# Kernel optimization log

Hardware: AMD Instinct MI355X
Metric: run time of the kernel (lower is better)

The kernel has to match this reference:

```python
import jax, jax.numpy as jnp
import numpy as np

B, N, D = 2, 2048, 1024
RANK, HEADS = 256, 16
HS = RANK // HEADS          # 16, low-rank head size for QK
DH = D // HEADS             # 64, value head size
SCALE = 1.0 / np.sqrt(HS)


def setup_inputs() -> dict:
    key = jax.random.key(0)
    k1, k2, k3 = jax.random.split(key, 3)
    x = jax.random.normal(k1, (B, N, D), dtype=jnp.float32)
    # causal additive mask, 0 on/below diag, -1e9 above
    mask = jnp.where(jnp.tril(jnp.ones((N, N), dtype=bool)), 0.0, -1e9).astype(jnp.float32)
    Wqk = jax.random.normal(k2, (2 * RANK, D), dtype=jnp.float32) * (1.0 / np.sqrt(D))
    Wv = jax.random.normal(k3, (D, D), dtype=jnp.float32) * (1.0 / np.sqrt(D))
    return {"x": x, "mask": mask, "Wqk": Wqk, "Wv": Wv}


def reference(x, mask, Wqk, Wv):
    b, n, d = x.shape
    qk = jnp.einsum('bnd,rd->bnr', x, Wqk)            # [b,n,2*rank]
    q, k = jnp.split(qk, 2, axis=-1)                  # [b,n,rank] each
    # L2 normalize over FULL rank dim (before head split), clamp norm >= 1e-6
    q = q / jnp.maximum(jnp.linalg.norm(q, axis=-1, keepdims=True), 1e-6)
    k = k / jnp.maximum(jnp.linalg.norm(k, axis=-1, keepdims=True), 1e-6)
    q = q.reshape(b, n, HEADS, HS).transpose(0, 2, 1, 3)   # [b,h,n,hs]
    k = k.reshape(b, n, HEADS, HS).transpose(0, 2, 1, 3)
    v = jnp.einsum('bnd,ed->bne', x, Wv).reshape(b, n, HEADS, DH).transpose(0, 2, 1, 3)  # [b,h,n,dh]
    att = jnp.einsum('bhqe,bhke->bhqk', q, k) * SCALE
    att = jnp.clip(att, -10000.0, 10000.0)
    att = att + mask[None, None, :, :]
    att = jax.nn.softmax(att, axis=-1)
    # NaN guard: zero NaNs then renormalize (no-op when no NaNs)
    att = jnp.where(jnp.isnan(att), 0.0, att)
    att = att / jnp.maximum(att.sum(axis=-1, keepdims=True), 1e-6)
    y = jnp.einsum('bhqk,bhkd->bhqd', att, v)              # [b,h,n,dh]
    return y.transpose(0, 2, 1, 3).reshape(b, n, d)
```

## Files before the change

### kernel.cpp

```cpp
#include <hip/hip_runtime.h>
#include <math.h>

#define BATCH 2
#define SEQ   2048
#define DIM   1024
#define RANK  256
#define HEADS 16
#define HS    16
#define DH    64
#define MROWS 4096

#define QSCALE 0.36067376f

typedef __attribute__((ext_vector_type(8)))  short    short8;
typedef __attribute__((ext_vector_type(4)))  float    f32x4;
typedef __attribute__((ext_vector_type(16))) float    f32x16;
typedef __attribute__((ext_vector_type(2)))  unsigned uint2v;

__device__ __forceinline__ unsigned short f2bf(float f) {
    union { float f; unsigned u; } v; v.f = f;
    return (unsigned short)((v.u + 0x7FFFu + ((v.u >> 16) & 1u)) >> 16);
}
__device__ __forceinline__ float bf2f(unsigned short h) {
    union { unsigned u; float f; } v; v.u = ((unsigned)h) << 16;
    return v.f;
}

#define XQ   1048576
#define WQKQ 131072
#define WVQ  262144
__global__ __launch_bounds__(256) void conv3(const float* __restrict__ x,
                                             const float* __restrict__ wqk,
                                             const float* __restrict__ wv,
                                             unsigned short* __restrict__ xb,
                                             unsigned short* __restrict__ wcat)
{
    const int i = blockIdx.x * 256 + threadIdx.x;
    const float* src; unsigned short* dst; int j;
    if (i < XQ)              { src = x;   dst = xb;   j = i; }
    else if (i < XQ + WQKQ)  { src = wqk; dst = wcat; j = i - XQ; }
    else                     { src = wv;  dst = wcat + (size_t)4 * WQKQ; j = i - XQ - WQKQ; }
    float4 v = ((const float4*)src)[j];
    ushort4 o; o.x = f2bf(v.x); o.y = f2bf(v.y); o.z = f2bf(v.z); o.w = f2bf(v.w);
    ((ushort4*)dst)[j] = o;
}

__global__ __launch_bounds__(256) void gemm_mfma(const unsigned short* __restrict__ A,
                                                 const unsigned short* __restrict__ W,
                                                 unsigned short* __restrict__ qkb,
                                                 unsigned short* __restrict__ vt)
{
    __shared__ __align__(16) unsigned short Alds[128 * 32];
    __shared__ __align__(16) unsigned short Blds[64 * 32];

    const int tid = threadIdx.x;
    const int w = tid >> 6, lane = tid & 63;
    const int lr = lane & 15, lg = lane >> 4;
    const int wm = w >> 1, wn = w & 1;
    const int bm = blockIdx.x * 128, bn = blockIdx.y * 64;

    const int srow = lane >> 2;
    const int sk   = (lane & 3) * 8;

    f32x4 acc[4][2] = {};

    for (int k0 = 0; k0 < 1024; k0 += 32) {
        __syncthreads();
        #pragma unroll
        for (int q = 0; q < 2; ++q) {
            const int r = (w * 2 + q) * 16 + srow;
            __builtin_amdgcn_global_load_lds(
                (const __attribute__((address_space(1))) unsigned int*)&A[(size_t)(bm + r) * 1024 + k0 + sk],
                (__attribute__((address_space(3))) unsigned int*)&Alds[(w * 2 + q) * 512],
                16, 0, 0);
        }
        __builtin_amdgcn_global_load_lds(
            (const __attribute__((address_space(1))) unsigned int*)&W[(size_t)(bn + w * 16 + srow) * 1024 + k0 + sk],
            (__attribute__((address_space(3))) unsigned int*)&Blds[w * 512],
            16, 0, 0);
        __syncthreads();

        short8 af[4], bfr[2];
        #pragma unroll
        for (int mi = 0; mi < 4; ++mi)
            af[mi] = *(const short8*)&Alds[(wm * 64 + mi * 16 + lr) * 32 + lg * 8];
        #pragma unroll
        for (int ni = 0; ni < 2; ++ni)
            bfr[ni] = *(const short8*)&Blds[(wn * 32 + ni * 16 + lr) * 32 + lg * 8];
        #pragma unroll
        for (int mi = 0; mi < 4; ++mi)
            #pragma unroll
            for (int ni = 0; ni < 2; ++ni)
                acc[mi][ni] = __builtin_amdgcn_mfma_f32_16x16x32_bf16(af[mi], bfr[ni], acc[mi][ni], 0, 0, 0);
    }

    if (bn < 512) {
        #pragma unroll
        for (int mi = 0; mi < 4; ++mi) {
            const int rbase = bm + wm * 64 + mi * 16 + lg * 4;
            #pragma unroll
            for (int ni = 0; ni < 2; ++ni) {
                const int col = bn + wn * 32 + ni * 16 + lr;
                #pragma unroll
                for (int r = 0; r < 4; ++r)
                    qkb[(size_t)(rbase + r) * 512 + col] = f2bf(acc[mi][ni][r]);
            }
        }
    } else {
        const int nb = bn - 512;
        #pragma unroll
        for (int mi = 0; mi < 4; ++mi) {
            const int m = bm + wm * 64 + mi * 16 + lg * 4;
            const int bb = m >> 11, ms = m & 2047;
            #pragma unroll
            for (int ni = 0; ni < 2; ++ni) {
                const int d = nb + wn * 32 + ni * 16 + lr;
                ushort4 pk;
                pk.x = f2bf(acc[mi][ni][0]); pk.y = f2bf(acc[mi][ni][1]);
                pk.z = f2bf(acc[mi][ni][2]); pk.w = f2bf(acc[mi][ni][3]);
                *(ushort4*)&vt[((size_t)bb * DIM + d) * SEQ + ms] = pk;
            }
        }
    }
}

__global__ __launch_bounds__(256) void l2norm_split(const unsigned short* __restrict__ qkb,
                                                    unsigned short* __restrict__ qn,
                                                    unsigned short* __restrict__ kn)
{
    const int row = blockIdx.x;
    const int t = threadIdx.x;
    const unsigned short* p = qkb + (size_t)row * 512;
    float q = bf2f(p[t]);
    float k = bf2f(p[t + 256]);
    float sq = q * q, sk = k * k;
    #pragma unroll
    for (int off = 32; off > 0; off >>= 1) {
        sq += __shfl_down(sq, off);
        sk += __shfl_down(sk, off);
    }
    __shared__ float sh[8];
    const int wid = t >> 6;
    if ((t & 63) == 0) { sh[wid * 2] = sq; sh[wid * 2 + 1] = sk; }
    __syncthreads();
    sq = sh[0] + sh[2] + sh[4] + sh[6];
    sk = sh[1] + sh[3] + sh[5] + sh[7];
    const float rq = QSCALE / fmaxf(sqrtf(sq), 1e-6f);
    const float rk = 1.0f   / fmaxf(sqrtf(sk), 1e-6f);
    qn[(size_t)row * 256 + t] = f2bf(q * rq);
    kn[(size_t)row * 256 + t] = f2bf(k * rk);
}


template<bool MASK>
__device__ __forceinline__ void tile32(const unsigned short* Vs, int keybase, int kh,
                                       int l31, int hi, int qg,
                                       const short8 ak0, const short8 ak1, const short8 bq,
                                       f32x16 o[2], float& lpart)
{
    const f32x16 z = {};
    const f32x16 s0 = __builtin_amdgcn_mfma_f32_32x32x16_bf16(ak0, bq, z, 0, 0, 0);
    const f32x16 s1 = __builtin_amdgcn_mfma_f32_32x32x16_bf16(ak1, bq, z, 0, 0, 0);

    float p0[16], p1[16];
    #pragma unroll
    for (int r = 0; r < 16; ++r) {
        float e0 = __builtin_exp2f(s0[r]);
        float e1 = __builtin_exp2f(s1[r]);
        if (MASK) {
            const int kl = keybase + (r & 3) + 8 * (r >> 2) + 4 * hi;
            e0 = (kl > qg) ? 0.0f : e0;
            e1 = (kl + 32 > qg) ? 0.0f : e1;
        }
        p0[r] = e0; p1[r] = e1;
        lpart += e0 + e1;
    }

    short8 pa[4];
    #pragma unroll
    for (int g = 0; g < 4; ++g) {
        const float* pc = (g < 2) ? p0 : p1;
        const int jj = 2 * (g & 1);
        unsigned a0, a1, b0, b1;
        asm("v_cvt_pk_bf16_f32 %0, %1, %2" : "=v"(a0) : "v"(pc[4*jj]),     "v"(pc[4*jj + 1]));
        asm("v_cvt_pk_bf16_f32 %0, %1, %2" : "=v"(b0) : "v"(pc[4*jj + 2]), "v"(pc[4*jj + 3]));
        asm("v_cvt_pk_bf16_f32 %0, %1, %2" : "=v"(a1) : "v"(pc[4*jj + 4]), "v"(pc[4*jj + 5]));
        asm("v_cvt_pk_bf16_f32 %0, %1, %2" : "=v"(b1) : "v"(pc[4*jj + 6]), "v"(pc[4*jj + 7]));
        const uint2v r0 = __builtin_amdgcn_permlane32_swap(a0, a1, false, false);
        const uint2v r1 = __builtin_amdgcn_permlane32_swap(b0, b1, false, false);
        union { short8 s; unsigned u[4]; } pu;
        pu.u[0] = r0[0]; pu.u[1] = r1[0]; pu.u[2] = r0[1]; pu.u[3] = r1[1];
        pa[g] = pu.s;
    }

    #pragma unroll
    for (int g = 0; g < 4; ++g)
        #pragma unroll
        for (int half = 0; half < 2; ++half) {
            const int row = half * 32 + l31;
            const short8 bv = *(const short8*)&Vs[row * 128 + ((64 * kh + 16 * g + 8 * hi) ^ (8 * (row & 7)))];
            o[half] = __builtin_amdgcn_mfma_f32_32x32x16_bf16(pa[g], bv, o[half], 0, 0, 0);
        }
}

__device__ __forceinline__ void seg_tile(const unsigned short* Vs, int kb, int kh,
                                         int l31, int hi, int qband, int qg, bool last,
                                         const short8 ak0, const short8 ak1, const short8 bq,
                                         f32x16 o[2], float& lpart)
{
    if (!last) {
        tile32<false>(Vs, kb, kh, l31, hi, qg, ak0, ak1, bq, o, lpart);
    } else if (kb <= qband + 31) {
        if (kb + 63 <= qband)
            tile32<false>(Vs, kb, kh, l31, hi, qg, ak0, ak1, bq, o, lpart);
        else
            tile32<true>(Vs, kb, kh, l31, hi, qg, ak0, ak1, bq, o, lpart);
    }
}

__global__ __launch_bounds__(256, 2) void attn_pair(const unsigned short* __restrict__ qn,
                                                    const unsigned short* __restrict__ kn,
                                                    const unsigned short* __restrict__ vt,
                                                    float* __restrict__ out)
{
    const int L = blockIdx.x;
    const int bh = L & 31;
    const int p  = L >> 5;
    const int h = bh & 15, b = bh >> 4;

    const int tid = threadIdx.x, w = tid >> 6, lane = tid & 63;
    const int qh = w >> 1, kh = w & 1;
    const int l31 = lane & 31, hi = lane >> 5;

    const int qt0 = 31 - p, qt1 = p;
    const int nt0 = (qt0 >> 1) + 1;
    const int nt1 = (qt1 >> 1) + 1;
    const int qband0 = qt0 * 64 + qh * 32, qband1 = qt1 * 64 + qh * 32;
    const int qg0 = qband0 + l31, qg1 = qband1 + l31;

    __shared__ __align__(16) unsigned char smem[33792];

    const short8 bq0 = *(const short8*)&qn[((size_t)b * SEQ + qg0) * RANK + h * HS + 8 * hi];
    const short8 bq1 = *(const short8*)&qn[((size_t)b * SEQ + qg1) * RANK + h * HS + 8 * hi];

    f32x16 o0[2] = {}, o1[2] = {};
    float lp0 = 0.0f, lp1 = 0.0f;

    const unsigned short* kbase = kn + ((size_t)b * SEQ + 64 * kh + l31) * RANK + h * HS + 8 * hi;
    short8 ak0 = *(const short8*)kbase;
    short8 ak1 = *(const short8*)(kbase + 32 * RANK);

    const int vsub  = lane >> 4;
    const int vslot = lane & 15;

#define STAGEV(kt_, buf_) do {                                                                    \
        const int k0_ = (kt_) * 128;                                                              \
        _Pragma("unroll")                                                                         \
        for (int i = 0; i < 4; ++i) {                                                             \
            const int dh = w * 16 + i * 4 + vsub;                                                 \
            const int so = 8 * (vslot ^ (dh & 7));                                                \
            __builtin_amdgcn_global_load_lds(                                                     \
                (const __attribute__((address_space(1))) unsigned int*)                           \
                    &vt[((size_t)b * DIM + h * DH + dh) * SEQ + k0_ + so],                        \
                (__attribute__((address_space(3))) unsigned int*)(smem + (buf_) * 16384 + (w * 4 + i) * 1024), \
                16, 0, 0);                                                                        \
        }                                                                                         \
    } while (0)

    STAGEV(0, 0);
    __syncthreads();

    #pragma unroll 1
    for (int kt = 0; kt < nt0; ++kt) {
        const bool more = (kt + 1 < nt0);
        if (more) STAGEV(kt + 1, (kt + 1) & 1);
        short8 an0 = ak0, an1 = ak1;
        if (more) {
            an0 = *(const short8*)(kbase + (size_t)(kt + 1) * 128 * RANK);
            an1 = *(const short8*)(kbase + (size_t)(kt + 1) * 128 * RANK + 32 * RANK);
        }

        const unsigned short* Vs = (const unsigned short*)(smem + (kt & 1) * 16384);
        const int kb = kt * 128 + 64 * kh;

        __builtin_amdgcn_s_setprio(1);
        seg_tile(Vs, kb, kh, l31, hi, qband0, qg0, kt == nt0 - 1, ak0, ak1, bq0, o0, lp0);
        if (kt < nt1)
            seg_tile(Vs, kb, kh, l31, hi, qband1, qg1, kt == nt1 - 1, ak0, ak1, bq1, o1, lp1);
        __builtin_amdgcn_s_setprio(0);

        ak0 = an0; ak1 = an1;
        __syncthreads();
    }
#undef STAGEV

    float* Os0 = (float*)smem;
    float* Os1 = (float*)(smem + 16384);
    float* Ls0 = (float*)(smem + 32768);
    float* Ls1 = (float*)(smem + 33280);

    if (kh == 1) {
        #pragma unroll
        for (int half = 0; half < 2; ++half)
            #pragma unroll
            for (int r = 0; r < 16; ++r) {
                const int q = (r & 3) + 8 * (r >> 2) + 4 * hi;
                Os0[(qh * 32 + q) * 64 + half * 32 + l31] = o0[half][r];
                Os1[(qh * 32 + q) * 64 + half * 32 + l31] = o1[half][r];
            }
        Ls0[qh * 64 + lane] = lp0;
        Ls1[qh * 64 + lane] = lp1;
    }
    __syncthreads();
    if (kh == 0) {
        float lt0 = lp0 + Ls0[qh * 64 + lane];
        float lt1 = lp1 + Ls1[qh * 64 + lane];
        lt0 += __shfl_xor(lt0, 32);
        lt1 += __shfl_xor(lt1, 32);
        const float inv0 = 1.0f / fmaxf(lt0, 1e-6f);
        const float inv1 = 1.0f / fmaxf(lt1, 1e-6f);
        #pragma unroll
        for (int r = 0; r < 16; ++r) {
            const int q = (r & 3) + 8 * (r >> 2) + 4 * hi;
            const float iv0 = __shfl(inv0, q);
            const float iv1 = __shfl(inv1, q);
            #pragma unroll
            for (int half = 0; half < 2; ++half) {
                const float v0 = (o0[half][r] + Os0[(qh * 32 + q) * 64 + half * 32 + l31]) * iv0;
                const float v1 = (o1[half][r] + Os1[(qh * 32 + q) * 64 + half * 32 + l31]) * iv1;
                __builtin_nontemporal_store(v0,
                    &out[((size_t)b * SEQ + qband0 + q) * DIM + h * DH + half * 32 + l31]);
                __builtin_nontemporal_store(v1,
                    &out[((size_t)b * SEQ + qband1 + q) * DIM + h * DH + half * 32 + l31]);
            }
        }
    }
}

extern "C" void kernel_launch(void* const* d_in, const int* in_sizes, int n_in,
                              void* d_out, int out_size, void* d_ws, size_t ws_size,
                              hipStream_t stream)
{
    const float* x   = (const float*)d_in[0];
    const float* Wqk = (const float*)d_in[2];
    const float* Wv  = (const float*)d_in[3];
    float* out = (float*)d_out;

    unsigned short* xb   = (unsigned short*)d_ws;
    unsigned short* qkb  = xb  + (size_t)MROWS * DIM;
    unsigned short* vt   = qkb + (size_t)MROWS * 512;
    unsigned short* wcat = vt  + (size_t)BATCH * DIM * SEQ;
    unsigned short* qn = xb;
    unsigned short* kn = xb + (size_t)MROWS * RANK;

    conv3<<<5632, 256, 0, stream>>>(x, Wqk, Wv, xb, wcat);
    gemm_mfma<<<dim3(32, 24), 256, 0, stream>>>(xb, wcat, qkb, vt);
    l2norm_split<<<MROWS, 256, 0, stream>>>(qkb, qn, kn);
    attn_pair<<<dim3(512), 256, 0, stream>>>(qn, kn, vt, out);
}
```

Before: 73.29 us.

## Widen GEMM K-tile with swizzled LDS, head-major QK layout, and finer attention sync

The projection GEMM now stages 64-wide K tiles into XOR-swizzled LDS, which halves the number of barrier iterations and avoids bank conflicts. Its grid is linearized and remapped so that blocks are grouped by chunk. The L2-norm kernel writes q and k in a head-major [b,h,n,16] layout so that attention reads K and Q contiguously. The attention loop replaces full syncthreads with an explicit vmcnt wait plus s_barrier, and preloads V fragments from LDS before the score MFMAs. Together these changes touch several kernels and carry more risk from hand-written waitcnt counts.

```diff
diff --git a/kernel.cpp b/kernel.cpp
--- a/kernel.cpp
+++ b/kernel.cpp
@@ -17,6 +17,9 @@
 typedef __attribute__((ext_vector_type(16))) float    f32x16;
 typedef __attribute__((ext_vector_type(2)))  unsigned uint2v;
 
+#define GPTR const __attribute__((address_space(1))) unsigned int*
+#define LPTR __attribute__((address_space(3))) unsigned int*
+
 __device__ __forceinline__ unsigned short f2bf(float f) {
     union { float f; unsigned u; } v; v.f = f;
     return (unsigned short)((v.u + 0x7FFFu + ((v.u >> 16) & 1u)) >> 16);
@@ -50,48 +53,60 @@
                                                  unsigned short* __restrict__ qkb,
                                                  unsigned short* __restrict__ vt)
 {
-    __shared__ __align__(16) unsigned short Alds[128 * 32];
-    __shared__ __align__(16) unsigned short Blds[64 * 32];
+    __shared__ __align__(16) unsigned short Alds[128 * 64];
+    __shared__ __align__(16) unsigned short Blds[64 * 64];
 
     const int tid = threadIdx.x;
     const int w = tid >> 6, lane = tid & 63;
     const int lr = lane & 15, lg = lane >> 4;
     const int wm = w >> 1, wn = w & 1;
-    const int bm = blockIdx.x * 128, bn = blockIdx.y * 64;
-
-    const int srow = lane >> 2;
-    const int sk   = (lane & 3) * 8;
+
+    const int Lf = blockIdx.x;
+    const int wg = (Lf & 7) * 96 + (Lf >> 3);
+    const int bm = (wg & 31) * 128;
+    const int bn = (wg >> 5) * 64;
+
+    const int rs = lane >> 3, cs = lane & 7;
 
     f32x4 acc[4][2] = {};
 
-    for (int k0 = 0; k0 < 1024; k0 += 32) {
+    for (int k0 = 0; k0 < 1024; k0 += 64) {
         __syncthreads();
         #pragma unroll
-        for (int q = 0; q < 2; ++q) {
-            const int r = (w * 2 + q) * 16 + srow;
+        for (int i = 0; i < 4; ++i) {
+            const int r = w * 32 + i * 8 + rs;
             __builtin_amdgcn_global_load_lds(
-                (const __attribute__((address_space(1))) unsigned int*)&A[(size_t)(bm + r) * 1024 + k0 + sk],
-                (__attribute__((address_space(3))) unsigned int*)&Alds[(w * 2 + q) * 512],
-                16, 0, 0);
-        }
-        __builtin_amdgcn_global_load_lds(
-            (const __attribute__((address_space(1))) unsigned int*)&W[(size_t)(bn + w * 16 + srow) * 1024 + k0 + sk],
-            (__attribute__((address_space(3))) unsigned int*)&Blds[w * 512],
-            16, 0, 0);
+                (GPTR)&A[(size_t)(bm + r) * 1024 + k0 + 8 * (cs ^ (r & 7))],
+                (LPTR)&Alds[(w * 32 + i * 8) * 64], 16, 0, 0);
+        }
+        #pragma unroll
+        for (int i = 0; i < 2; ++i) {
+            const int r = w * 16 + i * 8 + rs;
+            __builtin_amdgcn_global_load_lds(
+                (GPTR)&W[(size_t)(bn + r) * 1024 + k0 + 8 * (cs ^ (r & 7))],
+                (LPTR)&Blds[(w * 16 + i * 8) * 64], 16, 0, 0);
+        }
         __syncthreads();
 
-        short8 af[4], bfr[2];
-        #pragma unroll
-        for (int mi = 0; mi < 4; ++mi)
-            af[mi] = *(const short8*)&Alds[(wm * 64 + mi * 16 + lr) * 32 + lg * 8];
-        #pragma unroll
-        for (int ni = 0; ni < 2; ++ni)
-            bfr[ni] = *(const short8*)&Blds[(wn * 32 + ni * 16 + lr) * 32 + lg * 8];
-        #pragma unroll
-        for (int mi = 0; mi < 4; ++mi)
-            #pragma unroll
-            for (int ni = 0; ni < 2; ++ni)
-                acc[mi][ni] = __builtin_amdgcn_mfma_f32_16x16x32_bf16(af[mi], bfr[ni], acc[mi][ni], 0, 0, 0);
+        #pragma unroll
+        for (int kk = 0; kk < 2; ++kk) {
+            short8 af[4], bfr[2];
+            #pragma unroll
+            for (int mi = 0; mi < 4; ++mi) {
+                const int row = wm * 64 + mi * 16 + lr;
+                af[mi] = *(const short8*)&Alds[row * 64 + 8 * ((kk * 4 + lg) ^ (row & 7))];
+            }
+            #pragma unroll
+            for (int ni = 0; ni < 2; ++ni) {
+                const int row = wn * 32 + ni * 16 + lr;
+                bfr[ni] = *(const short8*)&Blds[row * 64 + 8 * ((kk * 4 + lg) ^ (row & 7))];
+            }
+            #pragma unroll
+            for (int mi = 0; mi < 4; ++mi)
+                #pragma unroll
+                for (int ni = 0; ni < 2; ++ni)
+                    acc[mi][ni] = __builtin_amdgcn_mfma_f32_16x16x32_bf16(af[mi], bfr[ni], acc[mi][ni], 0, 0, 0);
+        }
     }
 
     if (bn < 512) {
@@ -147,33 +162,31 @@
     sk = sh[1] + sh[3] + sh[5] + sh[7];
     const float rq = QSCALE / fmaxf(sqrtf(sq), 1e-6f);
     const float rk = 1.0f   / fmaxf(sqrtf(sk), 1e-6f);
-    qn[(size_t)row * 256 + t] = f2bf(q * rq);
-    kn[(size_t)row * 256 + t] = f2bf(k * rk);
+
+    const int b = row >> 11, n = row & 2047;
+    const int head = t >> 4, hs = t & 15;
+    const size_t o = (((size_t)b * HEADS + head) * SEQ + n) * 16 + hs;
+    qn[o] = f2bf(q * rq);
+    kn[o] = f2bf(k * rk);
 }
 
 
 template<bool MASK>
-__device__ __forceinline__ void tile32(const unsigned short* Vs, int keybase, int kh,
-                                       int l31, int hi, int qg,
-                                       const short8 ak0, const short8 ak1, const short8 bq,
-                                       f32x16 o[2], float& lpart)
-{
-    const f32x16 z = {};
-    const f32x16 s0 = __builtin_amdgcn_mfma_f32_32x32x16_bf16(ak0, bq, z, 0, 0, 0);
-    const f32x16 s1 = __builtin_amdgcn_mfma_f32_32x32x16_bf16(ak1, bq, z, 0, 0, 0);
-
+__device__ __forceinline__ void segpv(const f32x16& s0, const f32x16& s1, int kb, int hi,
+                                      int qg, const short8 vb[4][2], f32x16 o[2], float& lp)
+{
     float p0[16], p1[16];
     #pragma unroll
     for (int r = 0; r < 16; ++r) {
         float e0 = __builtin_exp2f(s0[r]);
         float e1 = __builtin_exp2f(s1[r]);
         if (MASK) {
-            const int kl = keybase + (r & 3) + 8 * (r >> 2) + 4 * hi;
+            const int kl = kb + (r & 3) + 8 * (r >> 2) + 4 * hi;
             e0 = (kl > qg) ? 0.0f : e0;
             e1 = (kl + 32 > qg) ? 0.0f : e1;
         }
         p0[r] = e0; p1[r] = e1;
-        lpart += e0 + e1;
+        lp += e0 + e1;
     }
 
     short8 pa[4];
@@ -196,32 +209,14 @@
     #pragma unroll
     for (int g = 0; g < 4; ++g)
         #pragma unroll
-        for (int half = 0; half < 2; ++half) {
-            const int row = half * 32 + l31;
-            const short8 bv = *(const short8*)&Vs[row * 128 + ((64 * kh + 16 * g + 8 * hi) ^ (8 * (row & 7)))];
-            o[half] = __builtin_amdgcn_mfma_f32_32x32x16_bf16(pa[g], bv, o[half], 0, 0, 0);
-        }
-}
-
-__device__ __forceinline__ void seg_tile(const unsigned short* Vs, int kb, int kh,
-                                         int l31, int hi, int qband, int qg, bool last,
-                                         const short8 ak0, const short8 ak1, const short8 bq,
-                                         f32x16 o[2], float& lpart)
-{
-    if (!last) {
-        tile32<false>(Vs, kb, kh, l31, hi, qg, ak0, ak1, bq, o, lpart);
-    } else if (kb <= qband + 31) {
-        if (kb + 63 <= qband)
-            tile32<false>(Vs, kb, kh, l31, hi, qg, ak0, ak1, bq, o, lpart);
-        else
-            tile32<true>(Vs, kb, kh, l31, hi, qg, ak0, ak1, bq, o, lpart);
-    }
-}
-
-__global__ __launch_bounds__(256, 2) void attn_pair(const unsigned short* __restrict__ qn,
-                                                    const unsigned short* __restrict__ kn,
-                                                    const unsigned short* __restrict__ vt,
-                                                    float* __restrict__ out)
+        for (int half = 0; half < 2; ++half)
+            o[half] = __builtin_amdgcn_mfma_f32_32x32x16_bf16(pa[g], vb[g][half], o[half], 0, 0, 0);
+}
+
+__global__ __launch_bounds__(256, 2) void attn_v2(const unsigned short* __restrict__ qn,
+                                                  const unsigned short* __restrict__ kn,
+                                                  const unsigned short* __restrict__ vt,
+                                                  float* __restrict__ out)
 {
     const int L = blockIdx.x;
     const int bh = L & 31;
@@ -240,18 +235,21 @@
 
     __shared__ __align__(16) unsigned char smem[33792];
 
-    const short8 bq0 = *(const short8*)&qn[((size_t)b * SEQ + qg0) * RANK + h * HS + 8 * hi];
-    const short8 bq1 = *(const short8*)&qn[((size_t)b * SEQ + qg1) * RANK + h * HS + 8 * hi];
+    const unsigned short* qbh = qn + (size_t)bh * SEQ * 16;
+    const unsigned short* kbh = kn + (size_t)bh * SEQ * 16;
+
+    const short8 bq0 = *(const short8*)&qbh[qg0 * 16 + 8 * hi];
+    const short8 bq1 = *(const short8*)&qbh[qg1 * 16 + 8 * hi];
 
     f32x16 o0[2] = {}, o1[2] = {};
     float lp0 = 0.0f, lp1 = 0.0f;
-
-    const unsigned short* kbase = kn + ((size_t)b * SEQ + 64 * kh + l31) * RANK + h * HS + 8 * hi;
-    short8 ak0 = *(const short8*)kbase;
-    short8 ak1 = *(const short8*)(kbase + 32 * RANK);
-
-    const int vsub  = lane >> 4;
-    const int vslot = lane & 15;
+    const f32x16 z = {};
+
+    const unsigned short* kwin = kbh + (64 * kh + l31) * 16 + 8 * hi;
+    short8 ak0 = *(const short8*)(kwin);
+    short8 ak1 = *(const short8*)(kwin + 32 * 16);
+
+    const int vsub = lane >> 4, vslot = lane & 15;
 
 #define STAGEV(kt_, buf_) do {                                                                    \
         const int k0_ = (kt_) * 128;                                                              \
@@ -260,40 +258,69 @@
             const int dh = w * 16 + i * 4 + vsub;                                                 \
             const int so = 8 * (vslot ^ (dh & 7));                                                \
             __builtin_amdgcn_global_load_lds(                                                     \
-                (const __attribute__((address_space(1))) unsigned int*)                           \
-                    &vt[((size_t)b * DIM + h * DH + dh) * SEQ + k0_ + so],                        \
-                (__attribute__((address_space(3))) unsigned int*)(smem + (buf_) * 16384 + (w * 4 + i) * 1024), \
-                16, 0, 0);                                                                        \
+                (GPTR)&vt[((size_t)b * DIM + h * DH + dh) * SEQ + k0_ + so],                      \
+                (LPTR)(smem + (buf_) * 16384 + (w * 4 + i) * 1024), 16, 0, 0);                    \
         }                                                                                         \
     } while (0)
 
     STAGEV(0, 0);
-    __syncthreads();
 
     #pragma unroll 1
     for (int kt = 0; kt < nt0; ++kt) {
-        const bool more = (kt + 1 < nt0);
-        if (more) STAGEV(kt + 1, (kt + 1) & 1);
         short8 an0 = ak0, an1 = ak1;
-        if (more) {
-            an0 = *(const short8*)(kbase + (size_t)(kt + 1) * 128 * RANK);
-            an1 = *(const short8*)(kbase + (size_t)(kt + 1) * 128 * RANK + 32 * RANK);
-        }
+        if (kt + 1 < nt0) {
+            STAGEV(kt + 1, (kt + 1) & 1);
+            an0 = *(const short8*)(kwin + (size_t)(kt + 1) * 128 * 16);
+            an1 = *(const short8*)(kwin + (size_t)(kt + 1) * 128 * 16 + 32 * 16);
+            asm volatile("s_waitcnt vmcnt(6)" ::: "memory");
+        } else {
+            asm volatile("s_waitcnt vmcnt(0)" ::: "memory");
+        }
+        __builtin_amdgcn_sched_barrier(0);
+        __builtin_amdgcn_s_barrier();
 
         const unsigned short* Vs = (const unsigned short*)(smem + (kt & 1) * 16384);
         const int kb = kt * 128 + 64 * kh;
 
+        short8 vb[4][2];
+        #pragma unroll
+        for (int g = 0; g < 4; ++g)
+            #pragma unroll
+            for (int half = 0; half < 2; ++half) {
+                const int row = half * 32 + l31;
+                const int slot = (8 * kh + 2 * g + hi) ^ (row & 7);
+                vb[g][half] = *(const short8*)&Vs[row * 128 + 8 * slot];
+            }
+
         __builtin_amdgcn_s_setprio(1);
-        seg_tile(Vs, kb, kh, l31, hi, qband0, qg0, kt == nt0 - 1, ak0, ak1, bq0, o0, lp0);
-        if (kt < nt1)
-            seg_tile(Vs, kb, kh, l31, hi, qband1, qg1, kt == nt1 - 1, ak0, ak1, bq1, o1, lp1);
+        if (kt < nt0 - 1) {
+            const f32x16 s0 = __builtin_amdgcn_mfma_f32_32x32x16_bf16(ak0, bq0, z, 0, 0, 0);
+            const f32x16 s1 = __builtin_amdgcn_mfma_f32_32x32x16_bf16(ak1, bq0, z, 0, 0, 0);
+            segpv<false>(s0, s1, kb, hi, qg0, vb, o0, lp0);
+        } else if (kb <= qband0 + 31) {
+            const f32x16 s0 = __builtin_amdgcn_mfma_f32_32x32x16_bf16(ak0, bq0, z, 0, 0, 0);
+            const f32x16 s1 = __builtin_amdgcn_mfma_f32_32x32x16_bf16(ak1, bq0, z, 0, 0, 0);
+            if (kb + 63 <= qband0) segpv<false>(s0, s1, kb, hi, qg0, vb, o0, lp0);
+            else                   segpv<true >(s0, s1, kb, hi, qg0, vb, o0, lp0);
+        }
+        if (kt < nt1) {
+            const f32x16 s0 = __builtin_amdgcn_mfma_f32_32x32x16_bf16(ak0, bq1, z, 0, 0, 0);
+            const f32x16 s1 = __builtin_amdgcn_mfma_f32_32x32x16_bf16(ak1, bq1, z, 0, 0, 0);
+            if (kt < nt1 - 1) {
+                segpv<false>(s0, s1, kb, hi, qg1, vb, o1, lp1);
+            } else if (kb <= qband1 + 31) {
+                if (kb + 63 <= qband1) segpv<false>(s0, s1, kb, hi, qg1, vb, o1, lp1);
+                else                   segpv<true >(s0, s1, kb, hi, qg1, vb, o1, lp1);
+            }
+        }
         __builtin_amdgcn_s_setprio(0);
 
         ak0 = an0; ak1 = an1;
-        __syncthreads();
+        __builtin_amdgcn_s_barrier();
     }
 #undef STAGEV
 
+    __syncthreads();
     float* Os0 = (float*)smem;
     float* Os1 = (float*)(smem + 16384);
     float* Ls0 = (float*)(smem + 32768);
@@ -351,10 +378,10 @@
     unsigned short* vt   = qkb + (size_t)MROWS * 512;
     unsigned short* wcat = vt  + (size_t)BATCH * DIM * SEQ;
     unsigned short* qn = xb;
-    unsigned short* kn = xb + (size_t)MROWS * RANK;
+    unsigned short* kn = xb + (size_t)32 * SEQ * 16;
 
     conv3<<<5632, 256, 0, stream>>>(x, Wqk, Wv, xb, wcat);
-    gemm_mfma<<<dim3(32, 24), 256, 0, stream>>>(xb, wcat, qkb, vt);
+    gemm_mfma<<<768, 256, 0, stream>>>(xb, wcat, qkb, vt);
     l2norm_split<<<MROWS, 256, 0, stream>>>(qkb, qn, kn);
-    attn_pair<<<dim3(512), 256, 0, stream>>>(qn, kn, vt, out);
-}
+    attn_v2<<<512, 256, 0, stream>>>(qn, kn, vt, out);
+}
```

New measurement: 70.56 us. 3.7% less time.
